# Kernel optimization log

Hardware: AMD Instinct MI355X
Metric: run time of the kernel (lower is better)

## Reference

```python
import jax, jax.numpy as jnp
import numpy as np

S, B, CIN, COUT, H, W, K = 4, 32, 128, 256, 16, 16, 3
D = CIN * K * K  # 1152, patch feature size = in_features
PRIOR_PREC = 1.0  # isotropic prior precision (prior_prec_full = PRIOR_PREC * I_D)
LOG_PREC_LR = 1.0


def _patches(x, k):
    # x: [N, C, H, W] -> [N, C*k*k, H, W]; channel-major patch ordering (matches torch unfold)
    pad = k // 2
    return jax.lax.conv_general_dilated_patches(
        x, (k, k), (1, 1), ((pad, pad), (pad, pad)),
        dimension_numbers=('NCHW', 'OIHW', 'NCHW'))


def setup_inputs() -> dict:
    key = jax.random.key(0)
    k1, k2, k3, k4 = jax.random.split(key, 4)
    X = jax.random.normal(k1, (S, B, CIN, H, W), jnp.float32)
    u = jax.random.normal(k2, (B, COUT, H, W), jnp.float32)
    log_prec_scaled = jax.random.normal(k3, (B,), jnp.float32)
    Z = jax.random.normal(k4, (S, COUT, D), jnp.float32)  # standard normal noise for rsample
    return {"X": X, "u": u, "log_prec_scaled": log_prec_scaled, "Z": Z}


def reference(X, u, log_prec_scaled, Z):
    Xi = X[:, :B]  # [S, B, CIN, H, W]
    sqrt_prec = jnp.exp(0.5 * LOG_PREC_LR * log_prec_scaled)[:, None, None, None]  # [B,1,1,1]
    Xil = sqrt_prec * Xi                     # [S, B, CIN, H, W]
    Yil = sqrt_prec * u                      # [B, COUT, H, W]

    # conv_mm: sufficient statistics via patch extraction
    P = _patches(Xil.reshape(S * B, CIN, H, W), K).reshape(S, B, D, H * W)
    Yf = Yil.reshape(B, COUT, H * W)
    XLX = jnp.einsum('sbdp,sbep->sde', P, P)       # [S, D, D]
    XLY = jnp.einsum('sbdp,bcp->sdc', P, Yf)       # [S, D, COUT]

    # rsample_logpq_weights
    prec = XLX + PRIOR_PREC * jnp.eye(D, dtype=XLX.dtype)   # [S, D, D]
    L = jnp.linalg.cholesky(prec)                            # [S, D, D], lower
    logdet_prec = 2.0 * jnp.sum(jnp.log(jnp.diagonal(L, axis1=-2, axis2=-1)), -1)  # [S]

    mu = jax.scipy.linalg.cho_solve((L, True), XLY)          # [S, D, COUT]
    # dW: solve L^T dW = Z (multi-RHS; L is shared across COUT)
    dW = jax.scipy.linalg.solve_triangular(L, jnp.swapaxes(Z, -1, -2), lower=True, trans='T')
    Wm = jnp.swapaxes(mu + dW, -1, -2)                       # [S, COUT, D]

    # logP: unnormalized MVN log-prob of each output neuron's weights under N(0, PRIOR_PREC^-1 I)
    logP = (0.5 * COUT * D * jnp.log(jnp.asarray(PRIOR_PREC, Wm.dtype))
            - 0.5 * PRIOR_PREC * jnp.sum(Wm * Wm, (-1, -2)))          # [S]
    logQ = -0.5 * jnp.sum(Z * Z, (-1, -2)) + 0.5 * COUT * logdet_prec  # [S]
    logpq = logP - logQ
    return Wm, logpq
```

## Files before the change

### kernel.cpp

```cpp
#include <hip/hip_runtime.h>
#include <math.h>

#define NS 4
#define NB 32
#define CIN 128
#define NCOUT 256
#define HWN 256
#define ND 1152
#define NK 8192
static const size_t D2 = (size_t)ND * ND;

typedef __attribute__((ext_vector_type(8))) short bf16x8;
typedef __attribute__((ext_vector_type(4))) float f32x4;

static __device__ inline unsigned short f2bf(float x) {
  unsigned int u = __float_as_uint(x);
  unsigned int r = (u + 0x7fffu + ((u >> 16) & 1u)) >> 16;
  return (unsigned short)r;
}
static __device__ inline float bf2f(unsigned short h) {
  return __uint_as_float(((unsigned int)h) << 16);
}
static __device__ inline float rdlane(float v, int l) {
  return __int_as_float(__builtin_amdgcn_readlane(__float_as_int(v), l));
}


__global__ void k_sqrtp(const float* __restrict__ lp, float* __restrict__ sp,
                        float* __restrict__ pp) {
  int b = threadIdx.x;
  if (b < NB) sp[b] = expf(0.5f * lp[b]);
  if (b < 8) pp[b] = 0.f;
}

__global__ __launch_bounds__(128) void k_patches(const float* __restrict__ X,
                                                 const float* __restrict__ sp,
                                                 unsigned short* __restrict__ Phi,
                                                 unsigned short* __restrict__ Plo) {
  int d = blockIdx.x, s = blockIdx.y, t = threadIdx.x;
  int c = d / 9, r = d % 9, ky = r / 3, kx = r % 3;
  int p0 = t * 2;
  int yy = (p0 >> 4) + ky - 1;
  int xx0 = (p0 & 15) + kx - 1;
  bool oky = (yy >= 0 && yy < 16);
  bool ok0 = oky && (xx0 >= 0) && (xx0 < 16);
  bool ok1 = oky && (xx0 + 1 >= 0) && (xx0 + 1 < 16);
  int xo = yy * 16 + xx0;
  size_t base = ((size_t)s * ND + d) * NK + p0;
  for (int b = 0; b < NB; ++b) {
    float sb = sp[b];
    const float* xb = X + ((size_t)(s * NB + b) * CIN + c) * HWN;
    float v0 = ok0 ? xb[xo] * sb : 0.f;
    float v1 = ok1 ? xb[xo + 1] * sb : 0.f;
    unsigned short h0 = f2bf(v0), h1 = f2bf(v1);
    unsigned short l0 = f2bf(v0 - bf2f(h0)), l1 = f2bf(v1 - bf2f(h1));
    size_t idx = base + (size_t)b * HWN;
    *(unsigned int*)(Phi + idx) = (unsigned int)h0 | ((unsigned int)h1 << 16);
    *(unsigned int*)(Plo + idx) = (unsigned int)l0 | ((unsigned int)l1 << 16);
  }
}

__global__ __launch_bounds__(128) void k_ytt(const float* __restrict__ u,
                                             const float* __restrict__ sp,
                                             unsigned short* __restrict__ Yhi,
                                             unsigned short* __restrict__ Ylo) {
  int c = blockIdx.x, t = threadIdx.x;
  int p0 = t * 2;
  for (int b = 0; b < NB; ++b) {
    float sb = sp[b];
    const float* ub = u + ((size_t)b * NCOUT + c) * HWN + p0;
    float v0 = ub[0] * sb, v1 = ub[1] * sb;
    unsigned short h0 = f2bf(v0), h1 = f2bf(v1);
    unsigned short l0 = f2bf(v0 - bf2f(h0)), l1 = f2bf(v1 - bf2f(h1));
    size_t idx = (size_t)c * NK + (size_t)b * HWN + p0;
    *(unsigned int*)(Yhi + idx) = (unsigned int)h0 | ((unsigned int)h1 << 16);
    *(unsigned int*)(Ylo + idx) = (unsigned int)l0 | ((unsigned int)l1 << 16);
  }
// ... 60 lines not shown
    __syncthreads();
    bf16x8 ah[4], al[4], bh[4], bl[4];
#pragma unroll
    for (int m = 0; m < 4; ++m) {
      int off = (arow0 + m * 16) * 32 + koff;
      ah[m] = *(const bf16x8*)&sAh[off];
      al[m] = *(const bf16x8*)&sAl[off];
    }
#pragma unroll
    for (int n = 0; n < 4; ++n) {
      int off = (brow0 + n * 16) * 32 + koff;
      bh[n] = *(const bf16x8*)&sBh[off];
      bl[n] = *(const bf16x8*)&sBl[off];
    }
#pragma unroll
    for (int m = 0; m < 4; ++m)
#pragma unroll
      for (int n = 0; n < 4; ++n) {
        acc[m][n] = __builtin_amdgcn_mfma_f32_16x16x32_bf16(ah[m], bh[n], acc[m][n], 0, 0, 0);
        acc[m][n] = __builtin_amdgcn_mfma_f32_16x16x32_bf16(ah[m], bl[n], acc[m][n], 0, 0, 0);
        acc[m][n] = __builtin_amdgcn_mfma_f32_16x16x32_bf16(al[m], bh[n], acc[m][n], 0, 0, 0);
      }
  }

  if (isX) {
    float* base = (kp ? prec2 : prec) + (size_t)s * D2;
#pragma unroll
    for (int m = 0; m < 4; ++m) {
      int row = i0 + wr * 64 + m * 16 + (lane >> 4) * 4;
#pragma unroll
      for (int n = 0; n < 4; ++n) {
        int col = j0 + wc * 64 + n * 16 + (lane & 15);
        float* cp = base + (size_t)row * ND + col;
#pragma unroll
        for (int r = 0; r < 4; ++r) cp[(size_t)r * ND] = acc[m][n][r];
      }
    }
  } else {
    float* base = (kp ? XLY2 : XLY) + (size_t)s * ND * NCOUT;
#pragma unroll
    for (int m = 0; m < 4; ++m) {
      int row = i0 + wr * 64 + m * 16 + (lane >> 4) * 4;
#pragma unroll
      for (int n = 0; n < 4; ++n) {
        int col = j0 + wc * 64 + n * 16 + (lane & 15);
        float* cp = base + (size_t)row * NCOUT + col;
#pragma unroll
        for (int r = 0; r < 4; ++r) cp[(size_t)r * NCOUT] = acc[m][n][r];
      }
    }
  }
}

__global__ __launch_bounds__(256, 3) void k_chol_dag(
    float* __restrict__ L, const float* __restrict__ Lp2,
    float* __restrict__ iA64, float* __restrict__ logd,
    int* __restrict__ flags) {
  int t0 = blockIdx.x, s = blockIdx.y;
  int bi = 0;
  while ((bi + 1) * (bi + 2) / 2 <= t0) ++bi;
  int bj = t0 - bi * (bi + 1) / 2;
  int ib = bi * 64, jb = bj * 64;
  float* Ls = L + (size_t)s * D2;
  const float* Ps = Lp2 + (size_t)s * D2;
  int* fc = flags + s * 324;

  __shared__ float At[64][68];
  __shared__ float Bt[64][68];
  int tid = threadIdx.x, tx = tid & 15, ty = tid >> 4;
  int lane = tid & 63, w = tid >> 6;

  float acc[4][4];
#pragma unroll
  for (int r = 0; r < 4; ++r) {
    size_t idx = (size_t)(ib + ty * 4 + r) * ND + jb + tx * 4;
    float4 v = *(const float4*)(Ls + idx);
    float4 v2 = *(const float4*)(Ps + idx);
    acc[r][0] = v.x + v2.x; acc[r][1] = v.y + v2.y;
    acc[r][2] = v.z + v2.z; acc[r][3] = v.w + v2.w;
  }
  if (bi == bj) {
#pragma unroll
    for (int r = 0; r < 4; ++r)
#pragma unroll
      for (int e = 0; e < 4; ++e)
        if (ty * 4 + r == tx * 4 + e) acc[r][e] += 1.f;
  }

  for (int k = 0; k < bj; ++k) {
    if (tid == 0) {
      while (__hip_atomic_load(&fc[bi * 18 + k], __ATOMIC_RELAXED,
                               __HIP_MEMORY_SCOPE_AGENT) == 0)
        __builtin_amdgcn_s_sleep(2);
      while (__hip_atomic_load(&fc[bj * 18 + k], __ATOMIC_RELAXED,
                               __HIP_MEMORY_SCOPE_AGENT) == 0)
        __builtin_amdgcn_s_sleep(2);
      (void)__hip_atomic_load(&fc[bj * 18 + k], __ATOMIC_ACQUIRE,
                              __HIP_MEMORY_SCOPE_AGENT);
    }
    __syncthreads();
    int kb = k * 64;
    {
      int a2 = tid >> 2, km = (tid & 3) * 4;
#pragma unroll
      for (int m = 0; m < 4; ++m) {
        float4 v = *(const float4*)(Ls + (size_t)(ib + a2) * ND + kb + km + m * 16);
        At[km + m * 16 + 0][a2] = v.x;
        At[km + m * 16 + 1][a2] = v.y;
        At[km + m * 16 + 2][a2] = v.z;
        At[km + m * 16 + 3][a2] = v.w;
        float4 u4 = *(const float4*)(Ls + (size_t)(jb + a2) * ND + kb + km + m * 16);
        Bt[km + m * 16 + 0][a2] = u4.x;
        Bt[km + m * 16 + 1][a2] = u4.y;
        Bt[km + m * 16 + 2][a2] = u4.z;
        Bt[km + m * 16 + 3][a2] = u4.w;
      }
    }
    __syncthreads();
#pragma unroll
    for (int kc = 0; kc < 64; ++kc) {
      float4 a4 = *(const float4*)&At[kc][ty * 4];
      float4 b4 = *(const float4*)&Bt[kc][tx * 4];
      float ar[4] = {a4.x, a4.y, a4.z, a4.w};
      float br[4] = {b4.x, b4.y, b4.z, b4.w};
#pragma unroll
      for (int r = 0; r < 4; ++r)
#pragma unroll
        for (int e = 0; e < 4; ++e) acc[r][e] = fmaf(-ar[r], br[e], acc[r][e]);
    }
    __syncthreads();
  }

  if (bi == bj) {
#pragma unroll
    for (int r = 0; r < 4; ++r)
#pragma unroll
      for (int e = 0; e < 4; ++e) At[ty * 4 + r][tx * 4 + e] = acc[r][e];
    {
      int rr = tid >> 2, cb2 = (tid & 3) * 16;
#pragma unroll
      for (int m = 0; m < 16; ++m) Bt[rr][cb2 + m] = (rr == cb2 + m) ? 1.f : 0.f;
    }
    __syncthreads();
    float diagv = 1.f;
    for (int p = 0; p < 8; ++p) {
      int c0 = p * 8;
      if (w == 0) {
        float pa[8], xb[8];
#pragma unroll
        for (int e = 0; e < 8; ++e) {
          pa[e] = At[lane][c0 + e];
          xb[e] = Bt[c0 + e][lane];
        }
#pragma unroll
        for (int j = 0; j < 8; ++j) {
          float dj = rdlane(pa[j], c0 + j);
          float r0 = __builtin_amdgcn_rsqf(dj);
          r0 = r0 * (1.5f - 0.5f * dj * r0 * r0);
          pa[j] *= r0;
          float xj = xb[j] * r0;
          xb[j] = xj;
          if (lane == c0 + j) diagv = dj * r0;
#pragma unroll
          for (int e = j + 1; e < 8; ++e) {
            float sv = rdlane(pa[j], c0 + e);
            pa[e] = fmaf(-pa[j], sv, pa[e]);
            xb[e] = fmaf(-sv, xj, xb[e]);
          }
        }
#pragma unroll
        for (int e = 0; e < 8; ++e) {
          At[lane][c0 + e] = pa[e];
          Bt[c0 + e][lane] = xb[e];
        }
      }
      __syncthreads();
      if (p < 7) {
        float La[8], Xp[8];
#pragma unroll
        for (int e = 0; e < 8; ++e) {
          La[e] = At[lane][c0 + e];
          Xp[e] = Bt[c0 + e][lane];
        }
        for (int c = c0 + 8 + w; c < 64; c += 4) {
          float Lc[8];
#pragma unroll
          for (int e = 0; e < 8; ++e) Lc[e] = At[c][c0 + e];
          float v = At[lane][c], vb = Bt[c][lane];
#pragma unroll
          for (int e = 0; e < 8; ++e) {
            v = fmaf(-La[e], Lc[e], v);
            vb = fmaf(-Lc[e], Xp[e], vb);
          }
          At[lane][c] = v;
          Bt[c][lane] = vb;
        }
        __syncthreads();
      }
    }
    if (w == 0) logd[s * ND + ib + lane] = logf(diagv);
    {
      float* q = iA64 + (size_t)(s * 18 + bi) * 4096;
      int rr = tid >> 2, cb2 = (tid & 3) * 16;
#pragma unroll
      for (int m = 0; m < 4; ++m)
        *(float4*)(q + rr * 64 + cb2 + m * 4) = *(const float4*)&Bt[rr][cb2 + m * 4];
    }
    __threadfence();
    __syncthreads();
    if (tid == 0)
      __hip_atomic_store(&fc[bi * 18 + bi], 1, __ATOMIC_RELEASE,
                         __HIP_MEMORY_SCOPE_AGENT);
  } else {
#pragma unroll
    for (int r = 0; r < 4; ++r)
#pragma unroll
      for (int e = 0; e < 4; ++e) At[tx * 4 + e][ty * 4 + r] = acc[r][e];
    __syncthreads();
    if (tid == 0) {
      while (__hip_atomic_load(&fc[bj * 18 + bj], __ATOMIC_RELAXED,
                               __HIP_MEMORY_SCOPE_AGENT) == 0)
        __builtin_amdgcn_s_sleep(2);
      (void)__hip_atomic_load(&fc[bj * 18 + bj], __ATOMIC_ACQUIRE,
                              __HIP_MEMORY_SCOPE_AGENT);
    }
    __syncthreads();
    {
      const float* q = iA64 + (size_t)(s * 18 + bj) * 4096;
      int a2 = tid >> 2, km = (tid & 3) * 4;
#pragma unroll
      for (int m = 0; m < 4; ++m) {
        float4 v = *(const float4*)(q + a2 * 64 + km + m * 16);
        Bt[km + m * 16 + 0][a2] = v.x;
        Bt[km + m * 16 + 1][a2] = v.y;
        Bt[km + m * 16 + 2][a2] = v.z;
        Bt[km + m * 16 + 3][a2] = v.w;
      }
    }
    __syncthreads();
    float acc2[4][4] = {};
#pragma unroll
    for (int kc = 0; kc < 64; ++kc) {
      float4 a4 = *(const float4*)&At[kc][ty * 4];
      float4 b4 = *(const float4*)&Bt[kc][tx * 4];
      float ar[4] = {a4.x, a4.y, a4.z, a4.w};
      float br[4] = {b4.x, b4.y, b4.z, b4.w};
#pragma unroll
      for (int r = 0; r < 4; ++r)
#pragma unroll
        for (int e = 0; e < 4; ++e) acc2[r][e] = fmaf(ar[r], br[e], acc2[r][e]);
    }
#pragma unroll
    for (int r = 0; r < 4; ++r) {
      float4 v = {acc2[r][0], acc2[r][1], acc2[r][2], acc2[r][3]};
      *(float4*)(Ls + (size_t)(ib + ty * 4 + r) * ND + jb + tx * 4) = v;
    }
    __threadfence();
    __syncthreads();
    if (tid == 0)
      __hip_atomic_store(&fc[bi * 18 + bj], 1, __ATOMIC_RELEASE,
                         __HIP_MEMORY_SCOPE_AGENT);
  }
}

__global__ __launch_bounds__(256) void k_invd128(const float* __restrict__ L,
                                                 const float* __restrict__ iA64,
                                                 float* __restrict__ iD) {
  int q = blockIdx.x, s = blockIdx.y;
  int tid = threadIdx.x;
  const float* Ls = L + (size_t)s * D2;
  float* out = iD + ((size_t)(s * 9 + q)) * 16384;
  int b0 = q * 128;
  __shared__ float inv0[64][68];
  __shared__ float invCt[64][68];
  __shared__ float Bt[64][68];
  __shared__ float Tl[64][68];

  {
    const float* iA0 = iA64 + (size_t)(s * 18 + 2 * q) * 4096;
    const float* iA1 = iA0 + 4096;
    int i = tid >> 2, c4 = (tid & 3) * 16;
#pragma unroll
    for (int m = 0; m < 4; ++m) {
      float4 v0 = *(const float4*)(iA0 + i * 64 + c4 + m * 4);
      *(float4*)&inv0[i][c4 + m * 4] = v0;
      float4 v1 = *(const float4*)(iA1 + i * 64 + c4 + m * 4);
      invCt[c4 + m * 4 + 0][i] = v1.x;
      invCt[c4 + m * 4 + 1][i] = v1.y;
      invCt[c4 + m * 4 + 2][i] = v1.z;
      invCt[c4 + m * 4 + 3][i] = v1.w;
    }
    const float* src = Ls + (size_t)(b0 + 64 + i) * ND + b0 + c4;
#pragma unroll
    for (int m = 0; m < 4; ++m) {
      float4 v = *(const float4*)(src + m * 4);
      Bt[c4 + m * 4 + 0][i] = v.x;
      Bt[c4 + m * 4 + 1][i] = v.y;
      Bt[c4 + m * 4 + 2][i] = v.z;
      Bt[c4 + m * 4 + 3][i] = v.w;
    }
  }
  __syncthreads();

  int tx = tid & 15, ty = tid >> 4;
  float acc[4][4] = {};
#pragma unroll
  for (int k = 0; k < 64; ++k) {
    float a4[4], b4[4];
#pragma unroll
    for (int e = 0; e < 4; ++e) { a4[e] = Bt[k][ty * 4 + e]; b4[e] = inv0[k][tx * 4 + e]; }
#pragma unroll
    for (int r = 0; r < 4; ++r)
#pragma unroll
      for (int e = 0; e < 4; ++e) acc[r][e] = fmaf(a4[r], b4[e], acc[r][e]);
  }
#pragma unroll
  for (int r = 0; r < 4; ++r)
#pragma unroll
    for (int e = 0; e < 4; ++e) Tl[ty * 4 + r][tx * 4 + e] = acc[r][e];
  __syncthreads();
  float acc2[4][4] = {};
#pragma unroll
  for (int k = 0; k < 64; ++k) {
    float a4[4], b4[4];
#pragma unroll
    for (int e = 0; e < 4; ++e) { a4[e] = invCt[k][ty * 4 + e]; b4[e] = Tl[k][tx * 4 + e]; }
#pragma unroll
    for (int r = 0; r < 4; ++r)
#pragma unroll
      for (int e = 0; e < 4; ++e) acc2[r][e] = fmaf(a4[r], b4[e], acc2[r][e]);
  }
  {
    int rrow = tid >> 2, cc = (tid & 3) * 32;
    float* o = out + rrow * 128 + cc;
    if (cc < 64) {
#pragma unroll
      for (int m = 0; m < 8; ++m) {
        float4 v = {inv0[rrow][cc + m * 4 + 0], inv0[rrow][cc + m * 4 + 1],
                    inv0[rrow][cc + m * 4 + 2], inv0[rrow][cc + m * 4 + 3]};
        *(float4*)(o + m * 4) = v;
      }
    } else {
      float4 z = {0.f, 0.f, 0.f, 0.f};
#pragma unroll
      for (int m = 0; m < 8; ++m) *(float4*)(o + m * 4) = z;
    }
  }
#pragma unroll
  for (int r = 0; r < 4; ++r) {
    float4 v = {-acc2[r][0], -acc2[r][1], -acc2[r][2], -acc2[r][3]};
    *(float4*)(out + (size_t)(64 + ty * 4 + r) * 128 + tx * 4) = v;
  }
  {
    int i = tid >> 2, jc = (tid & 3) * 16;
#pragma unroll
    for (int m = 0; m < 4; ++m) {
      float4 v = {invCt[jc + m * 4 + 0][i], invCt[jc + m * 4 + 1][i],
                  invCt[jc + m * 4 + 2][i], invCt[jc + m * 4 + 3][i]};
      *(float4*)(out + (size_t)(64 + i) * 128 + 64 + jc + m * 4) = v;
    }
  }
}

__global__ __launch_bounds__(256) void k_solve2(
    const float* __restrict__ L, const float* __restrict__ iD,
    const float* __restrict__ B1, const float* __restrict__ B2,
    const float* __restrict__ Z, float* __restrict__ Xf, float* __restrict__ Xb,
    float* __restrict__ Wm, float* __restrict__ pp, int* __restrict__ flags) {
  int r = blockIdx.x, ct = blockIdx.y, s = blockIdx.z;
  int rb = r * 128, cb = ct * 64;
  const float* Ls = L + (size_t)s * D2;
  const float* Dq = iD + ((size_t)(s * 9 + r)) * 16384;
  float* Xfs = Xf + (size_t)s * ND * NCOUT;
  float* Xbs = Xb + (size_t)s * ND * NCOUT;
  int fbf = 1296 + (s * 4 + ct) * 9;
  int fbb = 1440 + (s * 4 + ct) * 9;

  __shared__ float sA[32][132];
  __shared__ float sB[32][68];
  __shared__ float red[8];
  int tid = threadIdx.x, tx = tid & 15, ty = tid >> 4;
  int wave = tid >> 6, lane = tid & 63;

  float acc[8][4];
#pragma unroll
  for (int ii = 0; ii < 8; ++ii) {
    size_t idx = (size_t)s * ND * NCOUT + (size_t)(rb + ty * 8 + ii) * NCOUT + cb + tx * 4;
    float4 v = *(const float4*)(B1 + idx);
    float4 v2 = *(const float4*)(B2 + idx);
    acc[ii][0] = v.x + v2.x; acc[ii][1] = v.y + v2.y;
    acc[ii][2] = v.z + v2.z; acc[ii][3] = v.w + v2.w;
  }
  for (int q = 0; q < r; ++q) {
    if (tid == 0) {
      while (__hip_atomic_load(&flags[fbf + q], __ATOMIC_RELAXED,
                               __HIP_MEMORY_SCOPE_AGENT) == 0)
        __builtin_amdgcn_s_sleep(2);
      (void)__hip_atomic_load(&flags[fbf + q], __ATOMIC_ACQUIRE,
                              __HIP_MEMORY_SCOPE_AGENT);
    }
    __syncthreads();
    int qb = q * 128;
    for (int kk = 0; kk < 4; ++kk) {
      __syncthreads();
      {
        int i = tid >> 1, kb = (tid & 1) * 16;
        const float* src = Ls + (size_t)(rb + i) * ND + qb + kk * 32 + kb;
#pragma unroll
        for (int m = 0; m < 4; ++m) {
          float4 v = *(const float4*)(src + m * 4);
          sA[kb + m * 4 + 0][i] = v.x;
          sA[kb + m * 4 + 1][i] = v.y;
          sA[kb + m * 4 + 2][i] = v.z;
          sA[kb + m * 4 + 3][i] = v.w;
        }
      }
      {
        int k = tid >> 3, jb2 = (tid & 7) * 8;
        const float* src = Xfs + (size_t)(qb + kk * 32 + k) * NCOUT + cb + jb2;
        float4 v0 = *(const float4*)src;
        float4 v1 = *(const float4*)(src + 4);
        *(float4*)&sB[k][jb2] = v0;
        *(float4*)&sB[k][jb2 + 4] = v1;
      }
      __syncthreads();
#pragma unroll
      for (int k = 0; k < 32; ++k) {
        float4 a0 = *(const float4*)&sA[k][ty * 8];
        float4 a1 = *(const float4*)&sA[k][ty * 8 + 4];
        float4 b0 = *(const float4*)&sB[k][tx * 4];
        float a[8] = {a0.x, a0.y, a0.z, a0.w, a1.x, a1.y, a1.z, a1.w};
        float b[4] = {b0.x, b0.y, b0.z, b0.w};
#pragma unroll
        for (int ii = 0; ii < 8; ++ii)
#pragma unroll
          for (int j = 0; j < 4; ++j) acc[ii][j] = fmaf(-a[ii], b[j], acc[ii][j]);
      }
    }
  }
  float acc2[8][4] = {};
  for (int kk = 0; kk < 4; ++kk) {
    __syncthreads();
    if ((ty >> 2) == kk) {
      int kloc = ty * 8 - kk * 32;
#pragma unroll
      for (int ii = 0; ii < 8; ++ii) {
        float4 v = {acc[ii][0], acc[ii][1], acc[ii][2], acc[ii][3]};
        *(float4*)&sB[kloc + ii][tx * 4] = v;
      }
    }
    {
      int i = tid >> 1, kb = (tid & 1) * 16;
      const float* src = Dq + (size_t)i * 128 + kk * 32 + kb;
#pragma unroll
// ... 15 lines not shown
      float b[4] = {b0.x, b0.y, b0.z, b0.w};
#pragma unroll
      for (int ii = 0; ii < 8; ++ii)
#pragma unroll
        for (int j = 0; j < 4; ++j) acc2[ii][j] = fmaf(a[ii], b[j], acc2[ii][j]);
    }
  }
#pragma unroll
  for (int ii = 0; ii < 8; ++ii) {
    float4 v = {acc2[ii][0], acc2[ii][1], acc2[ii][2], acc2[ii][3]};
    *(float4*)(Xfs + (size_t)(rb + ty * 8 + ii) * NCOUT + cb + tx * 4) = v;
  }
  __threadfence();
  __syncthreads();
  if (tid == 0)
    __hip_atomic_store(&flags[fbf + r], 1, __ATOMIC_RELEASE,
                       __HIP_MEMORY_SCOPE_AGENT);

#pragma unroll
  for (int ii = 0; ii < 8; ++ii)
#pragma unroll
    for (int j = 0; j < 4; ++j) acc[ii][j] = acc2[ii][j];

  float zp = 0.f;
  for (int kk = 0; kk < 4; ++kk) {
    __syncthreads();
    {
      int c = tid >> 2, d8 = (tid & 3) * 8;
      const float* src = Z + ((size_t)(s * NCOUT) + cb + c) * ND + rb + kk * 32 + d8;
      float4 v0 = *(const float4*)src;
      float4 v1 = *(const float4*)(src + 4);
      sA[d8 + 0][c] = v0.x; sA[d8 + 1][c] = v0.y; sA[d8 + 2][c] = v0.z; sA[d8 + 3][c] = v0.w;
      sA[d8 + 4][c] = v1.x; sA[d8 + 5][c] = v1.y; sA[d8 + 6][c] = v1.z; sA[d8 + 7][c] = v1.w;
      zp += v0.x * v0.x + v0.y * v0.y + v0.z * v0.z + v0.w * v0.w;
      zp += v1.x * v1.x + v1.y * v1.y + v1.z * v1.z + v1.w * v1.w;
    }
    __syncthreads();
    if ((ty >> 2) == kk) {
      int kloc = ty * 8 - kk * 32;
#pragma unroll
      for (int ii = 0; ii < 8; ++ii) {
        float4 v = *(const float4*)&sA[kloc + ii][tx * 4];
        acc[ii][0] += v.x; acc[ii][1] += v.y; acc[ii][2] += v.z; acc[ii][3] += v.w;
      }
    }
  }
#pragma unroll
  for (int m2 = 32; m2 >= 1; m2 >>= 1) zp += __shfl_xor(zp, m2, 64);
  if (lane == 0) red[wave] = zp;
  __syncthreads();
  if (tid == 0) atomicAdd(pp + s, red[0] + red[1] + red[2] + red[3]);

  for (int q = 8; q > r; --q) {
    if (tid == 0) {
      while (__hip_atomic_load(&flags[fbb + q], __ATOMIC_RELAXED,
                               __HIP_MEMORY_SCOPE_AGENT) == 0)
        __builtin_amdgcn_s_sleep(2);
      (void)__hip_atomic_load(&flags[fbb + q], __ATOMIC_ACQUIRE,
                              __HIP_MEMORY_SCOPE_AGENT);
    }
    __syncthreads();
    int qb = q * 128;
    for (int kk = 0; kk < 4; ++kk) {
      __syncthreads();
      {
        int k = tid >> 3, ib2 = (tid & 7) * 16;
        const float* src = Ls + (size_t)(qb + kk * 32 + k) * ND + rb + ib2;
#pragma unroll
        for (int m = 0; m < 4; ++m)
          *(float4*)&sA[k][ib2 + m * 4] = *(const float4*)(src + m * 4);
      }
      {
        int k = tid >> 3, jb2 = (tid & 7) * 8;
        const float* src = Xbs + (size_t)(qb + kk * 32 + k) * NCOUT + cb + jb2;
        float4 v0 = *(const float4*)src;
        float4 v1 = *(const float4*)(src + 4);
        *(float4*)&sB[k][jb2] = v0;
        *(float4*)&sB[k][jb2 + 4] = v1;
      }
      __syncthreads();
#pragma unroll
      for (int k = 0; k < 32; ++k) {
        float4 a0 = *(const float4*)&sA[k][ty * 8];
        float4 a1 = *(const float4*)&sA[k][ty * 8 + 4];
        float4 b0 = *(const float4*)&sB[k][tx * 4];
        float a[8] = {a0.x, a0.y, a0.z, a0.w, a1.x, a1.y, a1.z, a1.w};
        float b[4] = {b0.x, b0.y, b0.z, b0.w};
#pragma unroll
        for (int ii = 0; ii < 8; ++ii)
#pragma unroll
          for (int j = 0; j < 4; ++j) acc[ii][j] = fmaf(-a[ii], b[j], acc[ii][j]);
      }
    }
  }
#pragma unroll
  for (int ii = 0; ii < 8; ++ii)
#pragma unroll
    for (int j = 0; j < 4; ++j) acc2[ii][j] = 0.f;
  for (int kk = 0; kk < 4; ++kk) {
    __syncthreads();
    if ((ty >> 2) == kk) {
      int kloc = ty * 8 - kk * 32;
#pragma unroll
      for (int ii = 0; ii < 8; ++ii) {
        float4 v = {acc[ii][0], acc[ii][1], acc[ii][2], acc[ii][3]};
        *(float4*)&sB[kloc + ii][tx * 4] = v;
      }
    }
    {
      int k = tid >> 3, ib2 = (tid & 7) * 16;
      const float* src = Dq + (size_t)(kk * 32 + k) * 128 + ib2;
#pragma unroll
      for (int m = 0; m < 4; ++m)
        *(float4*)&sA[k][ib2 + m * 4] = *(const float4*)(src + m * 4);
// ... 59 lines not shown
__global__ __launch_bounds__(256) void k_finalize(const float* __restrict__ logd,
                                                  const float* __restrict__ pp,
                                                  float* __restrict__ out) {
  int s = blockIdx.x, tid = threadIdx.x;
  __shared__ float r0[256];
  float l = 0.f;
  for (int i = tid; i < ND; i += 256) l += logd[s * ND + i];
  r0[tid] = l;
  __syncthreads();
  for (int off = 128; off; off >>= 1) {
    if (tid < off) r0[tid] += r0[tid + off];
    __syncthreads();
  }
  if (tid == 0) {
    float logdet = 2.0f * r0[0];
    out[s] = 0.5f * (pp[s] - pp[4 + s]) - 128.0f * logdet;
  }
}

extern "C" void kernel_launch(void* const* d_in, const int* in_sizes, int n_in,
                              void* d_out, int out_size, void* d_ws, size_t ws_size,
                              hipStream_t stream) {
  const float* X = (const float*)d_in[0];
  const float* u = (const float*)d_in[1];
  const float* lp = (const float*)d_in[2];
  const float* Z = (const float*)d_in[3];
  float* out = (float*)d_out;

  float* ws = (float*)d_ws;
  float* sp    = ws;
  float* invd  = sp + 64;
  float* logd  = invd + (size_t)NS * ND;
  float* pp    = logd + (size_t)NS * ND;
  int*   flags = (int*)(pp + 64);
  float* iD    = (float*)(flags + 2048);
  float* iA64  = iD + (size_t)NS * 9 * 16384;
  float* Xf    = iA64 + (size_t)NS * 18 * 4096;
  float* Xb    = Xf + (size_t)NS * ND * NCOUT;
  float* prec  = Xb + (size_t)NS * ND * NCOUT;
  float* prec2 = prec + (size_t)NS * D2;
  float* XLY   = prec2 + (size_t)NS * D2;
  float* XLY2  = XLY + (size_t)NS * ND * NCOUT;
  unsigned short* Phi = (unsigned short*)(XLY2 + (size_t)NS * ND * NCOUT);
  unsigned short* Plo = Phi + (size_t)NS * ND * NK;
  unsigned short* Yhi = Plo + (size_t)NS * ND * NK;
  unsigned short* Ylo = Yhi + (size_t)NCOUT * NK;

  hipMemsetAsync(flags, 0, 2048 * sizeof(int), stream);
  k_sqrtp<<<1, 64, 0, stream>>>(lp, sp, pp);
  k_patches<<<dim3(ND, NS), 128, 0, stream>>>(X, sp, Phi, Plo);
  k_ytt<<<NCOUT, 128, 0, stream>>>(u, sp, Yhi, Ylo);
  k_gemm_mfma<<<dim3(11, 9, NS * 2), 256, 0, stream>>>(Phi, Plo, Yhi, Ylo, prec,
                                                       prec2, XLY, XLY2);
  k_chol_dag<<<dim3(171, NS), 256, 0, stream>>>(prec, prec2, iA64, logd, flags);
  k_invd128<<<dim3(9, NS), 256, 0, stream>>>(prec, iA64, iD);
  k_solve2<<<dim3(9, 4, NS), 256, 0, stream>>>(prec, iD, XLY, XLY2, Z, Xf, Xb,
                                               out, pp, flags);
  k_finalize<<<NS, 256, 0, stream>>>(logd, pp, out + (size_t)NS * NCOUT * ND);
}
```

Before: 1.391 ms.

## Use 128-wide blocks in DAG Cholesky and fuse diagonal-block inversion into it

```diff
diff --git a/kernel.cpp b/kernel.cpp
--- a/kernel.cpp
+++ b/kernel.cpp
@@ -23,6 +23,20 @@
 }
 static __device__ inline float rdlane(float v, int l) {
   return __int_as_float(__builtin_amdgcn_readlane(__float_as_int(v), l));
+}
+static __device__ __forceinline__ void waitflag0(const int* f, int tid) {
+  if (tid == 0) {
+    while (__hip_atomic_load(f, __ATOMIC_RELAXED, __HIP_MEMORY_SCOPE_AGENT) == 0)
+      __builtin_amdgcn_s_sleep(2);
+    (void)__hip_atomic_load(f, __ATOMIC_ACQUIRE, __HIP_MEMORY_SCOPE_AGENT);
+  }
+  __syncthreads();
+}
+static __device__ __forceinline__ void publish0(int* f, int tid) {
+  __threadfence();
+  __syncthreads();
+  if (tid == 0)
+    __hip_atomic_store(f, 1, __ATOMIC_RELEASE, __HIP_MEMORY_SCOPE_AGENT);
 }
 
 
@@ -189,313 +203,347 @@
   }
 }
 
-__global__ __launch_bounds__(256, 3) void k_chol_dag(
+
+static __device__ __forceinline__ void factor64_core(
+    float* Af, float* Bf, int tid, int lane, int w, float* logdq) {
+  float (*At)[68] = (float(*)[68])Af;
+  float (*Bt)[68] = (float(*)[68])Bf;
+  {
+    int rr = tid >> 2, cb2 = (tid & 3) * 16;
+#pragma unroll
+    for (int m = 0; m < 16; ++m) Bt[rr][cb2 + m] = (rr == cb2 + m) ? 1.f : 0.f;
+  }
+  __syncthreads();
+  float diagv = 1.f;
+  for (int p = 0; p < 8; ++p) {
+    int c0 = p * 8;
+    if (w == 0) {
+      float pa[8], xb[8];
+#pragma unroll
+      for (int e = 0; e < 8; ++e) {
+        pa[e] = At[lane][c0 + e];
+        xb[e] = Bt[c0 + e][lane];
+      }
+#pragma unroll
+      for (int j = 0; j < 8; ++j) {
+        float dj = rdlane(pa[j], c0 + j);
+        float r0 = __builtin_amdgcn_rsqf(dj);
+        r0 = r0 * (1.5f - 0.5f * dj * r0 * r0);
+        pa[j] *= r0;
+        float xj = xb[j] * r0;
+        xb[j] = xj;
+        if (lane == c0 + j) diagv = dj * r0;
+#pragma unroll
+        for (int e = j + 1; e < 8; ++e) {
+          float sv = rdlane(pa[j], c0 + e);
+          pa[e] = fmaf(-pa[j], sv, pa[e]);
+          xb[e] = fmaf(-sv, xj, xb[e]);
+        }
+      }
+#pragma unroll
+      for (int e = 0; e < 8; ++e) {
+        At[lane][c0 + e] = pa[e];
+        Bt[c0 + e][lane] = xb[e];
+      }
+    }
+    __syncthreads();
+    if (p < 7) {
+      float La[8], Xp[8];
+#pragma unroll
+      for (int e = 0; e < 8; ++e) {
+        La[e] = At[lane][c0 + e];
+        Xp[e] = Bt[c0 + e][lane];
+      }
+      for (int c = c0 + 8 + w; c < 64; c += 4) {
+        float Lc[8];
+#pragma unroll
+        for (int e = 0; e < 8; ++e) Lc[e] = At[c][c0 + e];
+        float v = At[lane][c], vb = Bt[c][lane];
+#pragma unroll
+        for (int e = 0; e < 8; ++e) {
+          v = fmaf(-La[e], Lc[e], v);
+          vb = fmaf(-Lc[e], Xp[e], vb);
+        }
+        At[lane][c] = v;
+        Bt[c][lane] = vb;
+      }
+      __syncthreads();
+    }
+  }
+  if (w == 0) logdq[lane] = logf(diagv);
+  __syncthreads();
+}
+
+__global__ __launch_bounds__(256, 2) void k_chol_dag(
     float* __restrict__ L, const float* __restrict__ Lp2,
-    float* __restrict__ iA64, float* __restrict__ logd,
+    float* __restrict__ iD, float* __restrict__ logd,
     int* __restrict__ flags) {
   int t0 = blockIdx.x, s = blockIdx.y;
   int bi = 0;
   while ((bi + 1) * (bi + 2) / 2 <= t0) ++bi;
   int bj = t0 - bi * (bi + 1) / 2;
-  int ib = bi * 64, jb = bj * 64;
+  int ib = bi * 128, jb = bj * 128;
   float* Ls = L + (size_t)s * D2;
   const float* Ps = Lp2 + (size_t)s * D2;
-  int* fc = flags + s * 324;
-
-  __shared__ float At[64][68];
-  __shared__ float Bt[64][68];
+  int* fc = flags + s * 81;
+  float* iDo = iD + ((size_t)(s * 9 + bi)) * 16384;
+  const float* iDq = iD + ((size_t)(s * 9 + bj)) * 16384;
+
+  __shared__ float S[13056];
+  float* A64 = S;
+  float* B64 = S + 4352;
+  float* C64 = S + 8704;
+  float* SA = S;
+  float* SB = S + 4352;
+
   int tid = threadIdx.x, tx = tid & 15, ty = tid >> 4;
   int lane = tid & 63, w = tid >> 6;
 
-  float acc[4][4];
-#pragma unroll
-  for (int r = 0; r < 4; ++r) {
-    size_t idx = (size_t)(ib + ty * 4 + r) * ND + jb + tx * 4;
-    float4 v = *(const float4*)(Ls + idx);
-    float4 v2 = *(const float4*)(Ps + idx);
-    acc[r][0] = v.x + v2.x; acc[r][1] = v.y + v2.y;
-    acc[r][2] = v.z + v2.z; acc[r][3] = v.w + v2.w;
+  float acc[8][8];
+#pragma unroll
+  for (int rr = 0; rr < 8; ++rr) {
+    const float* p1 = Ls + (size_t)(ib + ty * 8 + rr) * ND + jb + tx * 8;
+    const float* p2 = Ps + (size_t)(ib + ty * 8 + rr) * ND + jb + tx * 8;
+    float4 v0 = *(const float4*)p1, v1 = *(const float4*)(p1 + 4);
+    float4 q0 = *(const float4*)p2, q1 = *(const float4*)(p2 + 4);
+    acc[rr][0] = v0.x + q0.x; acc[rr][1] = v0.y + q0.y;
+    acc[rr][2] = v0.z + q0.z; acc[rr][3] = v0.w + q0.w;
+    acc[rr][4] = v1.x + q1.x; acc[rr][5] = v1.y + q1.y;
+    acc[rr][6] = v1.z + q1.z; acc[rr][7] = v1.w + q1.w;
   }
   if (bi == bj) {
 #pragma unroll
-    for (int r = 0; r < 4; ++r)
-#pragma unroll
-      for (int e = 0; e < 4; ++e)
-        if (ty * 4 + r == tx * 4 + e) acc[r][e] += 1.f;
+    for (int rr = 0; rr < 8; ++rr)
+#pragma unroll
+      for (int e = 0; e < 8; ++e)
+        if (ty * 8 + rr == tx * 8 + e) acc[rr][e] += 1.f;
   }
 
   for (int k = 0; k < bj; ++k) {
     if (tid == 0) {
-      while (__hip_atomic_load(&fc[bi * 18 + k], __ATOMIC_RELAXED,
+      while (__hip_atomic_load(&fc[bi * 9 + k], __ATOMIC_RELAXED,
                                __HIP_MEMORY_SCOPE_AGENT) == 0)
         __builtin_amdgcn_s_sleep(2);
-      while (__hip_atomic_load(&fc[bj * 18 + k], __ATOMIC_RELAXED,
-                               __HIP_MEMORY_SCOPE_AGENT) == 0)
-        __builtin_amdgcn_s_sleep(2);
-      (void)__hip_atomic_load(&fc[bj * 18 + k], __ATOMIC_ACQUIRE,
+      if (bi != bj)
+        while (__hip_atomic_load(&fc[bj * 9 + k], __ATOMIC_RELAXED,
+                                 __HIP_MEMORY_SCOPE_AGENT) == 0)
+          __builtin_amdgcn_s_sleep(2);
+      (void)__hip_atomic_load(&fc[bi * 9 + k], __ATOMIC_ACQUIRE,
                               __HIP_MEMORY_SCOPE_AGENT);
     }
     __syncthreads();
-    int kb = k * 64;
-    {
-      int a2 = tid >> 2, km = (tid & 3) * 4;
-#pragma unroll
-      for (int m = 0; m < 4; ++m) {
-        float4 v = *(const float4*)(Ls + (size_t)(ib + a2) * ND + kb + km + m * 16);
-        At[km + m * 16 + 0][a2] = v.x;
-        At[km + m * 16 + 1][a2] = v.y;
-        At[km + m * 16 + 2][a2] = v.z;
-        At[km + m * 16 + 3][a2] = v.w;
-        float4 u4 = *(const float4*)(Ls + (size_t)(jb + a2) * ND + kb + km + m * 16);
-        Bt[km + m * 16 + 0][a2] = u4.x;
-        Bt[km + m * 16 + 1][a2] = u4.y;
-        Bt[km + m * 16 + 2][a2] = u4.z;
-        Bt[km + m * 16 + 3][a2] = u4.w;
-      }
-    }
-    __syncthreads();
-#pragma unroll
-    for (int kc = 0; kc < 64; ++kc) {
-      float4 a4 = *(const float4*)&At[kc][ty * 4];
-      float4 b4 = *(const float4*)&Bt[kc][tx * 4];
-      float ar[4] = {a4.x, a4.y, a4.z, a4.w};
-      float br[4] = {b4.x, b4.y, b4.z, b4.w};
-#pragma unroll
-      for (int r = 0; r < 4; ++r)
-#pragma unroll
-        for (int e = 0; e < 4; ++e) acc[r][e] = fmaf(-ar[r], br[e], acc[r][e]);
-    }
-    __syncthreads();
-  }
-
-  if (bi == bj) {
-#pragma unroll
-    for (int r = 0; r < 4; ++r)
-#pragma unroll
-      for (int e = 0; e < 4; ++e) At[ty * 4 + r][tx * 4 + e] = acc[r][e];
-    {
-      int rr = tid >> 2, cb2 = (tid & 3) * 16;
-#pragma unroll
-      for (int m = 0; m < 16; ++m) Bt[rr][cb2 + m] = (rr == cb2 + m) ? 1.f : 0.f;
-    }
-    __syncthreads();
-    float diagv = 1.f;
-    for (int p = 0; p < 8; ++p) {
-      int c0 = p * 8;
-      if (w == 0) {
-        float pa[8], xb[8];
-#pragma unroll
-        for (int e = 0; e < 8; ++e) {
-          pa[e] = At[lane][c0 + e];
-          xb[e] = Bt[c0 + e][lane];
+    for (int ks = 0; ks < 4; ++ks) {
+      __syncthreads();
+      {
+        int i = tid >> 1, kb = (tid & 1) * 16;
+        const float* sa = Ls + (size_t)(ib + i) * ND + k * 128 + ks * 32 + kb;
+#pragma unroll
+        for (int m = 0; m < 4; ++m) {
+          float4 v = *(const float4*)(sa + m * 4);
+          SA[(kb + m * 4 + 0) * 132 + i] = v.x;
+          SA[(kb + m * 4 + 1) * 132 + i] = v.y;
+          SA[(kb + m * 4 + 2) * 132 + i] = v.z;
+          SA[(kb + m * 4 + 3) * 132 + i] = v.w;
         }
-#pragma unroll
-        for (int j = 0; j < 8; ++j) {
-          float dj = rdlane(pa[j], c0 + j);
-          float r0 = __builtin_amdgcn_rsqf(dj);
-          r0 = r0 * (1.5f - 0.5f * dj * r0 * r0);
-          pa[j] *= r0;
-          float xj = xb[j] * r0;
-          xb[j] = xj;
-          if (lane == c0 + j) diagv = dj * r0;
-#pragma unroll
-          for (int e = j + 1; e < 8; ++e) {
-            float sv = rdlane(pa[j], c0 + e);
-            pa[e] = fmaf(-pa[j], sv, pa[e]);
-            xb[e] = fmaf(-sv, xj, xb[e]);
+        if (bi != bj) {
+          const float* sb = Ls + (size_t)(jb + i) * ND + k * 128 + ks * 32 + kb;
+#pragma unroll
+          for (int m = 0; m < 4; ++m) {
+            float4 v = *(const float4*)(sb + m * 4);
+            SB[(kb + m * 4 + 0) * 132 + i] = v.x;
+            SB[(kb + m * 4 + 1) * 132 + i] = v.y;
+            SB[(kb + m * 4 + 2) * 132 + i] = v.z;
+            SB[(kb + m * 4 + 3) * 132 + i] = v.w;
           }
         }
-#pragma unroll
-        for (int e = 0; e < 8; ++e) {
-          At[lane][c0 + e] = pa[e];
-          Bt[c0 + e][lane] = xb[e];
+      }
+      __syncthreads();
+      const float* SBu = (bi == bj) ? SA : SB;
+#pragma unroll
+      for (int kc = 0; kc < 32; ++kc) {
+        float4 a0 = *(const float4*)&SA[kc * 132 + ty * 8];
+        float4 a1 = *(const float4*)&SA[kc * 132 + ty * 8 + 4];
+        float4 b0 = *(const float4*)&SBu[kc * 132 + tx * 8];
+        float4 b1 = *(const float4*)&SBu[kc * 132 + tx * 8 + 4];
+        float a[8] = {a0.x, a0.y, a0.z, a0.w, a1.x, a1.y, a1.z, a1.w};
+        float b[8] = {b0.x, b0.y, b0.z, b0.w, b1.x, b1.y, b1.z, b1.w};
+#pragma unroll
+        for (int rr = 0; rr < 8; ++rr)
+#pragma unroll
+          for (int e = 0; e < 8; ++e) acc[rr][e] = fmaf(-a[rr], b[e], acc[rr][e]);
+      }
+    }
+  }
+
+  if (bi != bj) {
+    waitflag0(&fc[bj * 9 + bj], tid);
+    float c2[8][8];
+#pragma unroll
+    for (int rr = 0; rr < 8; ++rr)
+#pragma unroll
+      for (int e = 0; e < 8; ++e) c2[rr][e] = 0.f;
+    for (int ks = 0; ks < 4; ++ks) {
+      __syncthreads();
+      if ((tx >> 2) == ks) {
+#pragma unroll
+        for (int rr = 0; rr < 8; ++rr)
+#pragma unroll
+          for (int e = 0; e < 8; ++e)
+            SA[(tx * 8 + e - ks * 32) * 132 + ty * 8 + rr] = acc[rr][e];
+      }
+      {
+        int c = tid >> 1, kb = (tid & 1) * 16;
+        const float* sb = iDq + (size_t)c * 128 + ks * 32 + kb;
+#pragma unroll
+        for (int m = 0; m < 4; ++m) {
+          float4 v = *(const float4*)(sb + m * 4);
+          SB[(kb + m * 4 + 0) * 132 + c] = v.x;
+          SB[(kb + m * 4 + 1) * 132 + c] = v.y;
+          SB[(kb + m * 4 + 2) * 132 + c] = v.z;
+          SB[(kb + m * 4 + 3) * 132 + c] = v.w;
         }
       }
       __syncthreads();
-      if (p < 7) {
-        float La[8], Xp[8];
-#pragma unroll
-        for (int e = 0; e < 8; ++e) {
-          La[e] = At[lane][c0 + e];
-          Xp[e] = Bt[c0 + e][lane];
+#pragma unroll
+      for (int kc = 0; kc < 32; ++kc) {
+        float4 a0 = *(const float4*)&SA[kc * 132 + ty * 8];
+        float4 a1 = *(const float4*)&SA[kc * 132 + ty * 8 + 4];
+        float4 b0 = *(const float4*)&SB[kc * 132 + tx * 8];
+        float4 b1 = *(const float4*)&SB[kc * 132 + tx * 8 + 4];
+        float a[8] = {a0.x, a0.y, a0.z, a0.w, a1.x, a1.y, a1.z, a1.w};
+        float b[8] = {b0.x, b0.y, b0.z, b0.w, b1.x, b1.y, b1.z, b1.w};
+#pragma unroll
+        for (int rr = 0; rr < 8; ++rr)
+#pragma unroll
+          for (int e = 0; e < 8; ++e) c2[rr][e] = fmaf(a[rr], b[e], c2[rr][e]);
+      }
+    }
+#pragma unroll
+    for (int rr = 0; rr < 8; ++rr) {
+      float* dst = Ls + (size_t)(ib + ty * 8 + rr) * ND + jb + tx * 8;
+      float4 v0 = {c2[rr][0], c2[rr][1], c2[rr][2], c2[rr][3]};
+      float4 v1 = {c2[rr][4], c2[rr][5], c2[rr][6], c2[rr][7]};
+      *(float4*)dst = v0;
+      *(float4*)(dst + 4) = v1;
+    }
+    publish0(&fc[bi * 9 + bj], tid);
+  } else {
+    __syncthreads();
+    if (ty < 8 && tx < 8) {
+#pragma unroll
+      for (int rr = 0; rr < 8; ++rr)
+#pragma unroll
+        for (int e = 0; e < 8; ++e)
+          A64[(ty * 8 + rr) * 68 + tx * 8 + e] = acc[rr][e];
+    }
+    factor64_core(A64, B64, tid, lane, w, logd + (size_t)s * ND + ib);
+    {
+      int r = tid >> 2, c4 = (tid & 3) * 16;
+      float4 z = {0.f, 0.f, 0.f, 0.f};
+#pragma unroll
+      for (int m = 0; m < 4; ++m) {
+        *(float4*)(iDo + (size_t)r * 128 + c4 + m * 4) =
+            *(const float4*)&B64[r * 68 + c4 + m * 4];
+        *(float4*)(iDo + (size_t)r * 128 + 64 + c4 + m * 4) = z;
+      }
+    }
+    if (ty >= 8 && tx < 8) {
+#pragma unroll
+      for (int rr = 0; rr < 8; ++rr)
+#pragma unroll
+        for (int e = 0; e < 8; ++e)
+          A64[(tx * 8 + e) * 68 + (ty - 8) * 8 + rr] = acc[rr][e];
+    }
+    {
+      int r = tid >> 2, c4 = (tid & 3) * 16;
+#pragma unroll
+      for (int m = 0; m < 16; ++m)
+        C64[(c4 + m) * 68 + r] = B64[r * 68 + c4 + m];
+    }
+    __syncthreads();
+    float c21[4][4] = {};
+#pragma unroll
+    for (int kc = 0; kc < 64; ++kc) {
+      float4 a4 = *(const float4*)&A64[kc * 68 + ty * 4];
+      float4 b4 = *(const float4*)&C64[kc * 68 + tx * 4];
+      float a[4] = {a4.x, a4.y, a4.z, a4.w};
+      float b[4] = {b4.x, b4.y, b4.z, b4.w};
+#pragma unroll
+      for (int rr = 0; rr < 4; ++rr)
+#pragma unroll
+        for (int e = 0; e < 4; ++e) c21[rr][e] = fmaf(a[rr], b[e], c21[rr][e]);
+    }
+    __syncthreads();
+#pragma unroll
+    for (int rr = 0; rr < 4; ++rr)
+#pragma unroll
+      for (int e = 0; e < 4; ++e)
+        C64[(tx * 4 + e) * 68 + ty * 4 + rr] = c21[rr][e];
+    if (ty >= 8 && tx >= 8) {
+#pragma unroll
+      for (int rr = 0; rr < 8; ++rr)
+#pragma unroll
+        for (int e = 0; e < 8; ++e)
+          A64[((ty - 8) * 8 + rr) * 68 + (tx - 8) * 8 + e] = acc[rr][e];
+    }
+    __syncthreads();
+    float a22[4][4], m4[4][4] = {};
+#pragma unroll
+    for (int rr = 0; rr < 4; ++rr) {
+      float4 v = *(const float4*)&A64[(ty * 4 + rr) * 68 + tx * 4];
+      a22[rr][0] = v.x; a22[rr][1] = v.y; a22[rr][2] = v.z; a22[rr][3] = v.w;
+    }
+#pragma unroll
+    for (int kc = 0; kc < 64; ++kc) {
+      float4 a4 = *(const float4*)&C64[kc * 68 + ty * 4];
+      float4 b4 = *(const float4*)&C64[kc * 68 + tx * 4];
+      float4 g4 = *(const float4*)&B64[kc * 68 + tx * 4];
+      float a[4] = {a4.x, a4.y, a4.z, a4.w};
+      float b[4] = {b4.x, b4.y, b4.z, b4.w};
+      float g[4] = {g4.x, g4.y, g4.z, g4.w};
+#pragma unroll
+      for (int rr = 0; rr < 4; ++rr)
+#pragma unroll
+        for (int e = 0; e < 4; ++e) {
+          a22[rr][e] = fmaf(-a[rr], b[e], a22[rr][e]);
+          m4[rr][e] = fmaf(a[rr], g[e], m4[rr][e]);
         }
-        for (int c = c0 + 8 + w; c < 64; c += 4) {
-          float Lc[8];
-#pragma unroll
-          for (int e = 0; e < 8; ++e) Lc[e] = At[c][c0 + e];
-          float v = At[lane][c], vb = Bt[c][lane];
-#pragma unroll
-          for (int e = 0; e < 8; ++e) {
-            v = fmaf(-La[e], Lc[e], v);
-            vb = fmaf(-Lc[e], Xp[e], vb);
-          }
-          At[lane][c] = v;
-          Bt[c][lane] = vb;
-        }
-        __syncthreads();
-      }
-    }
-    if (w == 0) logd[s * ND + ib + lane] = logf(diagv);
+    }
+    __syncthreads();
+#pragma unroll
+    for (int rr = 0; rr < 4; ++rr) {
+      float4 va = {a22[rr][0], a22[rr][1], a22[rr][2], a22[rr][3]};
+      float4 vm = {m4[rr][0], m4[rr][1], m4[rr][2], m4[rr][3]};
+      *(float4*)&A64[(ty * 4 + rr) * 68 + tx * 4] = va;
+      *(float4*)&C64[(ty * 4 + rr) * 68 + tx * 4] = vm;
+    }
+    factor64_core(A64, B64, tid, lane, w, logd + (size_t)s * ND + ib + 64);
+    float i21[4][4] = {};
+#pragma unroll
+    for (int p = 0; p < 64; ++p) {
+      float a[4];
+#pragma unroll
+      for (int rr = 0; rr < 4; ++rr) a[rr] = B64[(ty * 4 + rr) * 68 + p];
+      float4 b4 = *(const float4*)&C64[p * 68 + tx * 4];
+      float b[4] = {b4.x, b4.y, b4.z, b4.w};
+#pragma unroll
+      for (int rr = 0; rr < 4; ++rr)
+#pragma unroll
+        for (int e = 0; e < 4; ++e) i21[rr][e] = fmaf(a[rr], b[e], i21[rr][e]);
+    }
+#pragma unroll
+    for (int rr = 0; rr < 4; ++rr) {
+      float4 v = {-i21[rr][0], -i21[rr][1], -i21[rr][2], -i21[rr][3]};
+      *(float4*)(iDo + (size_t)(64 + ty * 4 + rr) * 128 + tx * 4) = v;
+    }
     {
-      float* q = iA64 + (size_t)(s * 18 + bi) * 4096;
-      int rr = tid >> 2, cb2 = (tid & 3) * 16;
+      int r = tid >> 2, c4 = (tid & 3) * 16;
 #pragma unroll
       for (int m = 0; m < 4; ++m)
-        *(float4*)(q + rr * 64 + cb2 + m * 4) = *(const float4*)&Bt[rr][cb2 + m * 4];
-    }
-    __threadfence();
-    __syncthreads();
-    if (tid == 0)
-      __hip_atomic_store(&fc[bi * 18 + bi], 1, __ATOMIC_RELEASE,
-                         __HIP_MEMORY_SCOPE_AGENT);
-  } else {
-#pragma unroll
-    for (int r = 0; r < 4; ++r)
-#pragma unroll
-      for (int e = 0; e < 4; ++e) At[tx * 4 + e][ty * 4 + r] = acc[r][e];
-    __syncthreads();
-    if (tid == 0) {
-      while (__hip_atomic_load(&fc[bj * 18 + bj], __ATOMIC_RELAXED,
-                               __HIP_MEMORY_SCOPE_AGENT) == 0)
-        __builtin_amdgcn_s_sleep(2);
-      (void)__hip_atomic_load(&fc[bj * 18 + bj], __ATOMIC_ACQUIRE,
-                              __HIP_MEMORY_SCOPE_AGENT);
-    }
-    __syncthreads();
-    {
-      const float* q = iA64 + (size_t)(s * 18 + bj) * 4096;
-      int a2 = tid >> 2, km = (tid & 3) * 4;
-#pragma unroll
-      for (int m = 0; m < 4; ++m) {
-        float4 v = *(const float4*)(q + a2 * 64 + km + m * 16);
-        Bt[km + m * 16 + 0][a2] = v.x;
-        Bt[km + m * 16 + 1][a2] = v.y;
-        Bt[km + m * 16 + 2][a2] = v.z;
-        Bt[km + m * 16 + 3][a2] = v.w;
-      }
-    }
-    __syncthreads();
-    float acc2[4][4] = {};
-#pragma unroll
-    for (int kc = 0; kc < 64; ++kc) {
-      float4 a4 = *(const float4*)&At[kc][ty * 4];
-      float4 b4 = *(const float4*)&Bt[kc][tx * 4];
-      float ar[4] = {a4.x, a4.y, a4.z, a4.w};
-      float br[4] = {b4.x, b4.y, b4.z, b4.w};
-#pragma unroll
-      for (int r = 0; r < 4; ++r)
-#pragma unroll
-        for (int e = 0; e < 4; ++e) acc2[r][e] = fmaf(ar[r], br[e], acc2[r][e]);
-    }
-#pragma unroll
-    for (int r = 0; r < 4; ++r) {
-      float4 v = {acc2[r][0], acc2[r][1], acc2[r][2], acc2[r][3]};
-      *(float4*)(Ls + (size_t)(ib + ty * 4 + r) * ND + jb + tx * 4) = v;
-    }
-    __threadfence();
-    __syncthreads();
-    if (tid == 0)
-      __hip_atomic_store(&fc[bi * 18 + bj], 1, __ATOMIC_RELEASE,
-                         __HIP_MEMORY_SCOPE_AGENT);
-  }
-}
-
-__global__ __launch_bounds__(256) void k_invd128(const float* __restrict__ L,
-                                                 const float* __restrict__ iA64,
-                                                 float* __restrict__ iD) {
-  int q = blockIdx.x, s = blockIdx.y;
-  int tid = threadIdx.x;
-  const float* Ls = L + (size_t)s * D2;
-  float* out = iD + ((size_t)(s * 9 + q)) * 16384;
-  int b0 = q * 128;
-  __shared__ float inv0[64][68];
-  __shared__ float invCt[64][68];
-  __shared__ float Bt[64][68];
-  __shared__ float Tl[64][68];
-
-  {
-    const float* iA0 = iA64 + (size_t)(s * 18 + 2 * q) * 4096;
-    const float* iA1 = iA0 + 4096;
-    int i = tid >> 2, c4 = (tid & 3) * 16;
-#pragma unroll
-    for (int m = 0; m < 4; ++m) {
-      float4 v0 = *(const float4*)(iA0 + i * 64 + c4 + m * 4);
-      *(float4*)&inv0[i][c4 + m * 4] = v0;
-      float4 v1 = *(const float4*)(iA1 + i * 64 + c4 + m * 4);
-      invCt[c4 + m * 4 + 0][i] = v1.x;
-      invCt[c4 + m * 4 + 1][i] = v1.y;
-      invCt[c4 + m * 4 + 2][i] = v1.z;
-      invCt[c4 + m * 4 + 3][i] = v1.w;
-    }
-    const float* src = Ls + (size_t)(b0 + 64 + i) * ND + b0 + c4;
-#pragma unroll
-    for (int m = 0; m < 4; ++m) {
-      float4 v = *(const float4*)(src + m * 4);
-      Bt[c4 + m * 4 + 0][i] = v.x;
-      Bt[c4 + m * 4 + 1][i] = v.y;
-      Bt[c4 + m * 4 + 2][i] = v.z;
-      Bt[c4 + m * 4 + 3][i] = v.w;
-    }
-  }
-  __syncthreads();
-
-  int tx = tid & 15, ty = tid >> 4;
-  float acc[4][4] = {};
-#pragma unroll
-  for (int k = 0; k < 64; ++k) {
-    float a4[4], b4[4];
-#pragma unroll
-    for (int e = 0; e < 4; ++e) { a4[e] = Bt[k][ty * 4 + e]; b4[e] = inv0[k][tx * 4 + e]; }
-#pragma unroll
-    for (int r = 0; r < 4; ++r)
-#pragma unroll
-      for (int e = 0; e < 4; ++e) acc[r][e] = fmaf(a4[r], b4[e], acc[r][e]);
-  }
-#pragma unroll
-  for (int r = 0; r < 4; ++r)
-#pragma unroll
-    for (int e = 0; e < 4; ++e) Tl[ty * 4 + r][tx * 4 + e] = acc[r][e];
-  __syncthreads();
-  float acc2[4][4] = {};
-#pragma unroll
-  for (int k = 0; k < 64; ++k) {
-    float a4[4], b4[4];
-#pragma unroll
-    for (int e = 0; e < 4; ++e) { a4[e] = invCt[k][ty * 4 + e]; b4[e] = Tl[k][tx * 4 + e]; }
-#pragma unroll
-    for (int r = 0; r < 4; ++r)
-#pragma unroll
-      for (int e = 0; e < 4; ++e) acc2[r][e] = fmaf(a4[r], b4[e], acc2[r][e]);
-  }
-  {
-    int rrow = tid >> 2, cc = (tid & 3) * 32;
-    float* o = out + rrow * 128 + cc;
-    if (cc < 64) {
-#pragma unroll
-      for (int m = 0; m < 8; ++m) {
-        float4 v = {inv0[rrow][cc + m * 4 + 0], inv0[rrow][cc + m * 4 + 1],
-                    inv0[rrow][cc + m * 4 + 2], inv0[rrow][cc + m * 4 + 3]};
-        *(float4*)(o + m * 4) = v;
-      }
-    } else {
-      float4 z = {0.f, 0.f, 0.f, 0.f};
-#pragma unroll
-      for (int m = 0; m < 8; ++m) *(float4*)(o + m * 4) = z;
-    }
-  }
-#pragma unroll
-  for (int r = 0; r < 4; ++r) {
-    float4 v = {-acc2[r][0], -acc2[r][1], -acc2[r][2], -acc2[r][3]};
-    *(float4*)(out + (size_t)(64 + ty * 4 + r) * 128 + tx * 4) = v;
-  }
-  {
-    int i = tid >> 2, jc = (tid & 3) * 16;
-#pragma unroll
-    for (int m = 0; m < 4; ++m) {
-      float4 v = {invCt[jc + m * 4 + 0][i], invCt[jc + m * 4 + 1][i],
-                  invCt[jc + m * 4 + 2][i], invCt[jc + m * 4 + 3][i]};
-      *(float4*)(out + (size_t)(64 + i) * 128 + 64 + jc + m * 4) = v;
-    }
+        *(float4*)(iDo + (size_t)(64 + r) * 128 + 64 + c4 + m * 4) =
+            *(const float4*)&B64[r * 68 + c4 + m * 4];
+    }
+    publish0(&fc[bi * 9 + bi], tid);
   }
 }
 
@@ -529,14 +577,7 @@
     acc[ii][2] = v.z + v2.z; acc[ii][3] = v.w + v2.w;
   }
   for (int q = 0; q < r; ++q) {
-    if (tid == 0) {
-      while (__hip_atomic_load(&flags[fbf + q], __ATOMIC_RELAXED,
-                               __HIP_MEMORY_SCOPE_AGENT) == 0)
-        __builtin_amdgcn_s_sleep(2);
-      (void)__hip_atomic_load(&flags[fbf + q], __ATOMIC_ACQUIRE,
-                              __HIP_MEMORY_SCOPE_AGENT);
-    }
-    __syncthreads();
+    waitflag0(&flags[fbf + q], tid);
     int qb = q * 128;
     for (int kk = 0; kk < 4; ++kk) {
       __syncthreads();
@@ -658,14 +699,7 @@
   if (tid == 0) atomicAdd(pp + s, red[0] + red[1] + red[2] + red[3]);
 
   for (int q = 8; q > r; --q) {
-    if (tid == 0) {
-      while (__hip_atomic_load(&flags[fbb + q], __ATOMIC_RELAXED,
-                               __HIP_MEMORY_SCOPE_AGENT) == 0)
-        __builtin_amdgcn_s_sleep(2);
-      (void)__hip_atomic_load(&flags[fbb + q], __ATOMIC_ACQUIRE,
-                              __HIP_MEMORY_SCOPE_AGENT);
-    }
-    __syncthreads();
+    waitflag0(&flags[fbb + q], tid);
     int qb = q * 128;
     for (int kk = 0; kk < 4; ++kk) {
       __syncthreads();
@@ -831,8 +865,7 @@
   k_ytt<<<NCOUT, 128, 0, stream>>>(u, sp, Yhi, Ylo);
   k_gemm_mfma<<<dim3(11, 9, NS * 2), 256, 0, stream>>>(Phi, Plo, Yhi, Ylo, prec,
                                                        prec2, XLY, XLY2);
-  k_chol_dag<<<dim3(171, NS), 256, 0, stream>>>(prec, prec2, iA64, logd, flags);
-  k_invd128<<<dim3(9, NS), 256, 0, stream>>>(prec, iA64, iD);
+  k_chol_dag<<<dim3(45, NS), 256, 0, stream>>>(prec, prec2, iD, logd, flags);
   k_solve2<<<dim3(9, 4, NS), 256, 0, stream>>>(prec, iD, XLY, XLY2, Z, Xf, Xb,
                                                out, pp, flags);
   k_finalize<<<NS, 256, 0, stream>>>(logd, pp, out + (size_t)NS * NCOUT * ND);
```

Measured after the change: 2.122 ms. 52.5% more time.
